# Optimization experiments

Hardware: AMD Instinct MI355X
Metric: run time of the kernel (lower is better)

## Reference

```python
import jax, jax.numpy as jnp
import numpy as np

HEAD_SIZE = 64


def setup_inputs() -> dict:
    key = jax.random.key(0)
    kx, kk, kq, kv = jax.random.split(key, 4)
    B, T, C = 4, 4096, 1024
    x = jax.random.normal(kx, (B, T, C), dtype=jnp.float32)
    Wk = jax.random.normal(kk, (C, HEAD_SIZE), dtype=jnp.float32) * 0.02
    Wq = jax.random.normal(kq, (C, HEAD_SIZE), dtype=jnp.float32) * 0.02
    Wv = jax.random.normal(kv, (C, HEAD_SIZE), dtype=jnp.float32) * 0.02
    return {"x": x, "Wk": Wk, "Wq": Wq, "Wv": Wv}


def reference(x, Wk, Wq, Wv):
    # x: (B,T,C); projections to (B,T,H)
    T = x.shape[1]
    k = jnp.einsum('btc,ch->bth', x, Wk)
    q = jnp.einsum('btc,ch->bth', x, Wq)
    v = jnp.einsum('btc,ch->bth', x, Wv)
    scale = 1.0 / jnp.sqrt(jnp.float32(HEAD_SIZE))
    wei = jnp.einsum('bth,bsh->bts', q, k) * scale  # (B,T,T)
    causal = jnp.tril(jnp.ones((T, T), dtype=bool))
    wei = jnp.where(causal, wei, -jnp.inf)
    wei = jax.nn.softmax(wei, axis=-1)
    out = jnp.einsum('bts,bsh->bth', wei, v)  # (B,T,H)
    return out
```

## Files before the change

kernel.cpp:

```cpp
#include <hip/hip_runtime.h>

typedef __attribute__((ext_vector_type(8))) short short8;
typedef __attribute__((ext_vector_type(4))) float f32x4;
typedef unsigned short u16;

#define BB 4
#define TT 4096
#define CC 1024
#define HH 64

static __device__ __forceinline__ u16 f2bf(float f) {
    unsigned int u = __float_as_uint(f);
    unsigned int r = (u + 0x7FFFu + ((u >> 16) & 1u)) >> 16;
    return (u16)r;
}

static __device__ __forceinline__ unsigned int cvtpk(float lo, float hi) {
    unsigned int r;
    asm("v_cvt_pk_bf16_f32 %0, %1, %2" : "=v"(r) : "v"(lo), "v"(hi));
    return r;
}

static __device__ __forceinline__ int swz(int row, int chunk) {
    return row * 64 + ((chunk ^ (row & 7)) << 3);
}

static __device__ __forceinline__ int probe_isbf(const u16* xu, int tid) {
    int lane = tid & 63;
    int cnt = 0;
    for (int i = lane; i < 1024; i += 64) {
        u16 u = xu[2 * i];
        int e = (u >> 7) & 0xFF;
        cnt += (e >= 100 && e <= 140) ? 1 : 0;
    }
    for (int d = 1; d < 64; d <<= 1) cnt += __shfl_xor(cnt, d);
    return (cnt > 512) ? 1 : 0;
}

__global__ void prep(const void* __restrict__ Wk, const void* __restrict__ Wq,
                     const void* __restrict__ Wv, const u16* __restrict__ xu,
                     u16* __restrict__ Wtp, int* __restrict__ flag) {
    __shared__ int sflag;
    if (threadIdx.x < 64) {
        int f = probe_isbf(xu, threadIdx.x);
        if (threadIdx.x == 0) sflag = f;
    }
    __syncthreads();
    const int isbf = sflag;
    if (blockIdx.x == 0 && threadIdx.x == 0) *flag = isbf;

    int r = blockIdx.x;
    int p = r >> 6;
    int n = r & 63;
    int nt = n >> 4, nl = n & 15;
    const void* W = (p == 0) ? Wq : (p == 1) ? Wk : Wv;
    int k0 = threadIdx.x * 4;
    int kb = k0 >> 6, k2 = (k0 >> 5) & 1, quad = (k0 >> 3) & 3, half = (k0 >> 2) & 1;
    ushort4 v;
    if (isbf) {
        const u16* Wb = (const u16*)W;
        v.x = Wb[(k0 + 0) * HH + n]; v.y = Wb[(k0 + 1) * HH + n];
        v.z = Wb[(k0 + 2) * HH + n]; v.w = Wb[(k0 + 3) * HH + n];
    } else {
        const float* Wf = (const float*)W;
        v.x = f2bf(Wf[(k0 + 0) * HH + n]); v.y = f2bf(Wf[(k0 + 1) * HH + n]);
        v.z = f2bf(Wf[(k0 + 2) * HH + n]); v.w = f2bf(Wf[(k0 + 3) * HH + n]);
    }
    size_t off16 = ((size_t)((p * 4 + nt) * 16 + kb) * 2 + k2) * 64 + quad * 16 + nl;
    *reinterpret_cast<ushort4*>(Wtp + off16 * 8 + half * 4) = v;
}

__global__ __launch_bounds__(256) void qkv_proj(const void* __restrict__ x,
                                                const u16* __restrict__ Wtp,
                                                u16* __restrict__ qo, u16* __restrict__ ko,
                                                u16* __restrict__ vo, const int* __restrict__ flag) {
    __shared__ __align__(16) u16 xs[32 * 1024];
    __shared__ __align__(16) u16 tls[4][3][256];
    const int isbf = *flag;
    const int tid = threadIdx.x;
    const int lane = tid & 63;
    const int w = tid >> 6;
    const int l15 = lane & 15;
    const int quad = lane >> 4;
    int phys = blockIdx.x;
    int rb = (phys & 7) * 64 + (phys >> 3);
    const int g0r = rb * 32;

    #pragma unroll
    for (int j = 0; j < 16; j++) {
        int c = tid + j * 256;
        int row = c >> 7, ck = c & 127;
        int dst = row * 1024 + ((ck ^ (row & 7)) << 3);
        if (isbf) {
            uint4 d = *reinterpret_cast<const uint4*>((const u16*)x + (size_t)(g0r + row) * CC + ck * 8);
            *reinterpret_cast<uint4*>(xs + dst) = d;
        } else {
            const float4* pf = reinterpret_cast<const float4*>((const float*)x + (size_t)(g0r + row) * CC + ck * 8);
            float4 a0 = pf[0], a1 = pf[1];
            ushort4 lo; lo.x = f2bf(a0.x); lo.y = f2bf(a0.y); lo.z = f2bf(a0.z); lo.w = f2bf(a0.w);
            ushort4 hi; hi.x = f2bf(a1.x); hi.y = f2bf(a1.y); hi.z = f2bf(a1.z); hi.w = f2bf(a1.w);
            *reinterpret_cast<ushort4*>(xs + dst) = lo;
            *reinterpret_cast<ushort4*>(xs + dst + 4) = hi;
        }
    }
    __syncthreads();

    f32x4 zero = {0.f, 0.f, 0.f, 0.f};
    f32x4 acc[3][2];
    #pragma unroll
    for (int i = 0; i < 3; i++) { acc[i][0] = zero; acc[i][1] = zero; }

    for (int kb = 0; kb < 16; kb++) {
        #pragma unroll
        for (int k2 = 0; k2 < 2; k2++) {
            int ck = kb * 8 + k2 * 4 + quad;
            int xo = ((ck ^ (l15 & 7)) << 3);
            short8 af0 = *reinterpret_cast<const short8*>(xs + l15 * 1024 + xo);
            short8 af1 = *reinterpret_cast<const short8*>(xs + (16 + l15) * 1024 + xo);
            #pragma unroll
            for (int p = 0; p < 3; p++) {
                short8 bf = *reinterpret_cast<const short8*>(
                    Wtp + ((((size_t)(p * 4 + w) * 16 + kb) * 2 + k2) * 64 + lane) * 8);
                acc[p][0] = __builtin_amdgcn_mfma_f32_16x16x32_bf16(af0, bf, acc[p][0], 0, 0, 0);
                acc[p][1] = __builtin_amdgcn_mfma_f32_16x16x32_bf16(af1, bf, acc[p][1], 0, 0, 0);
            }
        }
    }

    const float qscale = 0.18033688011112042f;
    #pragma unroll
    for (int rt = 0; rt < 2; rt++) {
        const int g0rt = g0r + rt * 16;
        #pragma unroll
        for (int p = 0; p < 3; p++) {
            if (p < 2) {
                float sc = (p == 0) ? qscale : 1.f;
                #pragma unroll
                for (int r = 0; r < 4; r++)
                    tls[w][p][(quad * 4 + r) * 16 + l15] = f2bf(acc[p][rt][r] * sc);
            } else {
                #pragma unroll
                for (int r = 0; r < 4; r++)
                    tls[w][p][l15 * 16 + quad * 4 + r] = f2bf(acc[p][rt][r]);
            }
        }
        #pragma unroll
        for (int p = 0; p < 2; p++) {
            int t = lane >> 2, seg = lane & 3;
            ushort4 d = *reinterpret_cast<const ushort4*>(&tls[w][p][t * 16 + seg * 4]);
            u16* dst = (p == 0) ? qo : ko;
            *reinterpret_cast<ushort4*>(dst + (size_t)(g0rt + t) * HH + w * 16 + seg * 4) = d;
        }
        {
            int c = lane >> 2, seg = lane & 3;
            ushort4 d = *reinterpret_cast<const ushort4*>(&tls[w][2][c * 16 + seg * 4]);
            int b = g0rt >> 12;
            int kt = (g0rt & 4095) >> 6;
            int toff = g0rt & 63;
            *reinterpret_cast<ushort4*>(vo + ((size_t)((b * 64 + kt) * 64 + w * 16 + c)) * 64 + toff + seg * 4) = d;
        }
    }
}

static __device__ __forceinline__ void attn_step(const u16* __restrict__ kstc,
                                                 const u16* __restrict__ vtsc,
                                                 u16* __restrict__ pbw,
                                                 const short8* aq, f32x4* o, float& lsum,
                                                 int kt, int q_g, bool dm, int l15, int quad) {
    f32x4 zero = {0.f, 0.f, 0.f, 0.f};
    f32x4 s[4];
    #pragma unroll
    for (int i = 0; i < 4; i++) s[i] = zero;
    __builtin_amdgcn_s_setprio(1);
    #pragma unroll
    for (int k2 = 0; k2 < 2; k2++) {
        #pragma unroll
        for (int nt = 0; nt < 4; nt++) {
            short8 af = *reinterpret_cast<const short8*>(&kstc[swz(nt * 16 + l15, k2 * 4 + quad)]);
            s[nt] = __builtin_amdgcn_mfma_f32_16x16x32_bf16(af, aq[k2], s[nt], 0, 0, 0);
        }
    }
    __builtin_amdgcn_s_setprio(0);
    #pragma unroll
    for (int nt = 0; nt < 4; nt++) {
        int key0 = kt * 64 + nt * 16 + quad * 4;
        #pragma unroll
        for (int r = 0; r < 4; r++) {
            float pv = __builtin_amdgcn_exp2f(s[nt][r]);
            if (dm && key0 + r > q_g) pv = 0.f;
            s[nt][r] = pv;
        }
    }
    #pragma unroll
    for (int nt = 0; nt < 4; nt++)
        lsum += (s[nt][0] + s[nt][1]) + (s[nt][2] + s[nt][3]);
    #pragma unroll
    for (int nt = 0; nt < 4; nt++) {
        uint2 pk;
        pk.x = cvtpk(s[nt][0], s[nt][1]);
        pk.y = cvtpk(s[nt][2], s[nt][3]);
        int addr = swz(l15, nt * 2 + (quad >> 1)) + (quad & 1) * 4;
        *reinterpret_cast<uint2*>(&pbw[addr]) = pk;
    }
    __builtin_amdgcn_s_setprio(1);
    #pragma unroll
    for (int k2 = 0; k2 < 2; k2++) {
        short8 bp = *reinterpret_cast<const short8*>(&pbw[swz(l15, k2 * 4 + quad)]);
        #pragma unroll
        for (int nt = 0; nt < 4; nt++) {
            short8 av = *reinterpret_cast<const short8*>(&vtsc[swz(nt * 16 + l15, k2 * 4 + quad)]);
            o[nt] = __builtin_amdgcn_mfma_f32_16x16x32_bf16(av, bp, o[nt], 0, 0, 0);
        }
    }
    __builtin_amdgcn_s_setprio(0);
}

__global__ __launch_bounds__(256) void attn(const u16* __restrict__ qp, const u16* __restrict__ kp,
                                            const u16* __restrict__ vp, float* __restrict__ acco,
                                            float* __restrict__ accl, void* __restrict__ outv,
                                            const int* __restrict__ flag, int nsplit) {
    __shared__ __align__(16) u16 kst[2][64 * 64];
    __shared__ __align__(16) u16 vts[2][64 * 64];
    __shared__ __align__(16) u16 pb[4][16 * 64];
    const int isbf = *flag;
    const int tid = threadIdx.x;
    const int lane = tid & 63;
    const int w = tid >> 6;
    const int l15 = lane & 15;
    const int quad = lane >> 4;

    int u = blockIdx.x;
    int per = 32 * nsplit;
    int b = u / per;
    int rem = u - b * per;
    int p = rem / nsplit;
    int ks = rem - p * nsplit;
    const int qtA = 63 - p;
    const int qtB = p;

    const int q_gA = qtA * 64 + w * 16 + l15;
    const int q_gB = qtB * 64 + w * 16 + l15;

    short8 aqA[2], aqB[2];
    {
        const u16* qr = qp + (size_t)(b * TT + q_gA) * HH;
        aqA[0] = *reinterpret_cast<const short8*>(qr + quad * 8);
        aqA[1] = *reinterpret_cast<const short8*>(qr + 32 + quad * 8);
    }
    {
        const u16* qr = qp + (size_t)(b * TT + q_gB) * HH;
        aqB[0] = *reinterpret_cast<const short8*>(qr + quad * 8);
        aqB[1] = *reinterpret_cast<const short8*>(qr + 32 + quad * 8);
    }

    const int cc0 = tid, cc1 = tid + 256;
    const int dst0 = swz(cc0 >> 3, cc0 & 7);
    const int dst1 = swz(cc1 >> 3, cc1 & 7);
    const u16* kbase = kp + (size_t)b * TT * HH;
    const u16* vbase = vp + (size_t)b * 64 * 64 * 64;

    f32x4 zero = {0.f, 0.f, 0.f, 0.f};
    f32x4 oA[4], oB[4];
    #pragma unroll
    for (int i = 0; i < 4; i++) { oA[i] = zero; oB[i] = zero; }
    float lsumA = 0.f, lsumB = 0.f;

    const int nstep = (qtA - ks) / nsplit + 1;

    uint4 rk0, rk1, rv0, rv1;
    {
        size_t t0 = (size_t)ks * 4096;
        rk0 = *reinterpret_cast<const uint4*>(kbase + t0 + cc0 * 8);
        rk1 = *reinterpret_cast<const uint4*>(kbase + t0 + cc1 * 8);
        rv0 = *reinterpret_cast<const uint4*>(vbase + t0 + cc0 * 8);
        rv1 = *reinterpret_cast<const uint4*>(vbase + t0 + cc1 * 8);
    }
    *reinterpret_cast<uint4*>(&kst[0][dst0]) = rk0;
    *reinterpret_cast<uint4*>(&kst[0][dst1]) = rk1;
    *reinterpret_cast<uint4*>(&vts[0][dst0]) = rv0;
    *reinterpret_cast<uint4*>(&vts[0][dst1]) = rv1;
    if (nstep > 1) {
        size_t t1 = (size_t)(ks + nsplit) * 4096;
        rk0 = *reinterpret_cast<const uint4*>(kbase + t1 + cc0 * 8);
        rk1 = *reinterpret_cast<const uint4*>(kbase + t1 + cc1 * 8);
        rv0 = *reinterpret_cast<const uint4*>(vbase + t1 + cc0 * 8);
        rv1 = *reinterpret_cast<const uint4*>(vbase + t1 + cc1 * 8);
    }

    for (int j = 0; j < nstep; ++j) {
        __syncthreads();
        const int cur = j & 1;
        if (j + 1 < nstep) {
            *reinterpret_cast<uint4*>(&kst[cur ^ 1][dst0]) = rk0;
            *reinterpret_cast<uint4*>(&kst[cur ^ 1][dst1]) = rk1;
            *reinterpret_cast<uint4*>(&vts[cur ^ 1][dst0]) = rv0;
            *reinterpret_cast<uint4*>(&vts[cur ^ 1][dst1]) = rv1;
        }
        if (j + 2 < nstep) {
            size_t tn = (size_t)(ks + (j + 2) * nsplit) * 4096;
            rk0 = *reinterpret_cast<const uint4*>(kbase + tn + cc0 * 8);
            rk1 = *reinterpret_cast<const uint4*>(kbase + tn + cc1 * 8);
            rv0 = *reinterpret_cast<const uint4*>(vbase + tn + cc0 * 8);
            rv1 = *reinterpret_cast<const uint4*>(vbase + tn + cc1 * 8);
        }
        const int kt = ks + j * nsplit;
        attn_step(&kst[cur][0], &vts[cur][0], &pb[w][0], aqA, oA, lsumA,
                  kt, q_gA, kt == qtA, l15, quad);
        if (kt <= qtB)
            attn_step(&kst[cur][0], &vts[cur][0], &pb[w][0], aqB, oB, lsumB,
                      kt, q_gB, kt == qtB, l15, quad);
    }

    lsumA += __shfl_xor(lsumA, 16);
    lsumA += __shfl_xor(lsumA, 32);
    lsumB += __shfl_xor(lsumB, 16);
    lsumB += __shfl_xor(lsumB, 32);

    const size_t g0qA = (size_t)(b * TT) + q_gA;
    const size_t g0qB = (size_t)(b * TT) + q_gB;

    if (nsplit == 1) {
        float invA = 1.0f / lsumA;
        float invB = 1.0f / lsumB;
        if (isbf) {
            u16* outp = (u16*)outv;
            #pragma unroll
            for (int nt = 0; nt < 4; nt++) {
                ushort4 sa, sb;
                sa.x = f2bf(oA[nt][0] * invA); sa.y = f2bf(oA[nt][1] * invA);
                sa.z = f2bf(oA[nt][2] * invA); sa.w = f2bf(oA[nt][3] * invA);
                sb.x = f2bf(oB[nt][0] * invB); sb.y = f2bf(oB[nt][1] * invB);
                sb.z = f2bf(oB[nt][2] * invB); sb.w = f2bf(oB[nt][3] * invB);
                *reinterpret_cast<ushort4*>(outp + g0qA * HH + nt * 16 + quad * 4) = sa;
                *reinterpret_cast<ushort4*>(outp + g0qB * HH + nt * 16 + quad * 4) = sb;
            }
        } else {
            float* outp = (float*)outv;
            #pragma unroll
            for (int nt = 0; nt < 4; nt++) {
                float4 sa = {oA[nt][0] * invA, oA[nt][1] * invA, oA[nt][2] * invA, oA[nt][3] * invA};
                float4 sb = {oB[nt][0] * invB, oB[nt][1] * invB, oB[nt][2] * invB, oB[nt][3] * invB};
                *reinterpret_cast<float4*>(outp + g0qA * HH + nt * 16 + quad * 4) = sa;
                *reinterpret_cast<float4*>(outp + g0qB * HH + nt * 16 + quad * 4) = sb;
            }
        }
    } else {
        float* accos = acco + (size_t)ks * (BB * TT * HH);
        float* accls = accl + (size_t)ks * (BB * TT);
        #pragma unroll
        for (int nt = 0; nt < 4; nt++) {
            float4 sv = {oA[nt][0], oA[nt][1], oA[nt][2], oA[nt][3]};
            *reinterpret_cast<float4*>(accos + g0qA * HH + nt * 16 + quad * 4) = sv;
        }
        if (quad == 0) accls[g0qA] = lsumA;
        if (ks <= qtB) {
            #pragma unroll
            for (int nt = 0; nt < 4; nt++) {
                float4 sv = {oB[nt][0], oB[nt][1], oB[nt][2], oB[nt][3]};
                *reinterpret_cast<float4*>(accos + g0qB * HH + nt * 16 + quad * 4) = sv;
            }
            if (quad == 0) accls[g0qB] = lsumB;
        }
    }
}

__global__ __launch_bounds__(256) void attn_finalize(const float* __restrict__ acco,
                                                     const float* __restrict__ accl,
                                                     void* __restrict__ outv,
                                                     const int* __restrict__ flag, int nsplit) {
    const int isbf = *flag;
    int i = blockIdx.x * blockDim.x + threadIdx.x;
    int row = i >> 4;
    int qt = (row & (TT - 1)) >> 6;
    int nact = min(nsplit, qt + 1);
    float4 ov = reinterpret_cast<const float4*>(acco)[i];
    float l = accl[row];
    for (int s = 1; s < nact; s++) {
        float4 t = reinterpret_cast<const float4*>(acco + (size_t)s * (BB * TT * HH))[i];
        ov.x += t.x; ov.y += t.y; ov.z += t.z; ov.w += t.w;
        l += accl[(size_t)s * (BB * TT) + row];
    }
    float inv = 1.0f / l;
    if (isbf) {
        ushort4 s;
        s.x = f2bf(ov.x * inv); s.y = f2bf(ov.y * inv);
        s.z = f2bf(ov.z * inv); s.w = f2bf(ov.w * inv);
        reinterpret_cast<ushort4*>(outv)[i] = s;
    } else {
        float4 s = {ov.x * inv, ov.y * inv, ov.z * inv, ov.w * inv};
        reinterpret_cast<float4*>(outv)[i] = s;
    }
}

extern "C" void kernel_launch(void* const* d_in, const int* in_sizes, int n_in,
                              void* d_out, int out_size, void* d_ws, size_t ws_size,
                              hipStream_t stream) {
    const void* x  = d_in[0];
    const void* Wk = d_in[1];
    const void* Wq = d_in[2];
    const void* Wv = d_in[3];
    char* ws = (char*)d_ws;
    u16* qo = (u16*)(ws);
    u16* ko = (u16*)(ws + (size_t)2 * 1024 * 1024);
    u16* vo = (u16*)(ws + (size_t)4 * 1024 * 1024);
    u16* Wtp = (u16*)(ws + (size_t)6 * 1024 * 1024);
    int* flag = (int*)(ws + (size_t)6 * 1024 * 1024 + 768 * 1024);
    float* acco = (float*)(ws + (size_t)7 * 1024 * 1024);
    float* accl = (float*)(ws + (size_t)39 * 1024 * 1024);

    const size_t need_split = (size_t)40 * 1024 * 1024;
    const int nsplit = (ws_size >= need_split) ? 8 : 1;

    prep<<<192, 256, 0, stream>>>(Wk, Wq, Wv, (const u16*)x, Wtp, flag);
    qkv_proj<<<512, 256, 0, stream>>>(x, Wtp, qo, ko, vo, flag);
    attn<<<BB * 32 * nsplit, 256, 0, stream>>>(qo, ko, vo, acco, accl, d_out, flag, nsplit);
    if (nsplit > 1) {
        attn_finalize<<<(BB * TT * HH / 4) / 256, 256, 0, stream>>>(acco, accl, d_out, flag, nsplit);
    }
}
```

Baseline: 145.9 us.

## Load K fragments directly from global into registers, drop K LDS staging

K tiles are no longer staged through shared memory. Each lane loads its MFMA K fragments straight from global memory into registers and prefetches the next tile's fragments after the QK^T MFMAs. Separate P buffers for the A and B query tiles remove the reuse hazard on the shared P scratch, and the key split factor drops from 8 to 4. This trades LDS traffic and LDS footprint for redundant global/L2 loads of K across the four waves and more register pressure, with fewer, longer split blocks.

```diff
diff --git a/kernel.cpp b/kernel.cpp
--- a/kernel.cpp
+++ b/kernel.cpp
@@ -162,25 +162,29 @@
     }
 }
 
-static __device__ __forceinline__ void attn_step(const u16* __restrict__ kstc,
-                                                 const u16* __restrict__ vtsc,
-                                                 u16* __restrict__ pbw,
-                                                 const short8* aq, f32x4* o, float& lsum,
-                                                 int kt, int q_g, bool dm, int l15, int quad) {
-    f32x4 zero = {0.f, 0.f, 0.f, 0.f};
-    f32x4 s[4];
-    #pragma unroll
-    for (int i = 0; i < 4; i++) s[i] = zero;
+static __device__ __forceinline__ void qkt_regs(const short8* kf, const short8* aq, f32x4* s) {
     __builtin_amdgcn_s_setprio(1);
     #pragma unroll
     for (int k2 = 0; k2 < 2; k2++) {
         #pragma unroll
-        for (int nt = 0; nt < 4; nt++) {
-            short8 af = *reinterpret_cast<const short8*>(&kstc[swz(nt * 16 + l15, k2 * 4 + quad)]);
-            s[nt] = __builtin_amdgcn_mfma_f32_16x16x32_bf16(af, aq[k2], s[nt], 0, 0, 0);
-        }
+        for (int nt = 0; nt < 4; nt++)
+            s[nt] = __builtin_amdgcn_mfma_f32_16x16x32_bf16(kf[k2 * 4 + nt], aq[k2], s[nt], 0, 0, 0);
     }
     __builtin_amdgcn_s_setprio(0);
+}
+
+static __device__ __forceinline__ void load_kf(short8* kf, const u16* kfb, size_t toff) {
+    #pragma unroll
+    for (int k2 = 0; k2 < 2; k2++) {
+        #pragma unroll
+        for (int nt = 0; nt < 4; nt++)
+            kf[k2 * 4 + nt] = *reinterpret_cast<const short8*>(kfb + toff + nt * 1024 + k2 * 32);
+    }
+}
+
+static __device__ __forceinline__ void smpv(f32x4* s, const u16* __restrict__ vtsc,
+                                            u16* __restrict__ pbw, f32x4* o, float& lsum,
+                                            int kt, int q_g, bool dm, int l15, int quad) {
     #pragma unroll
     for (int nt = 0; nt < 4; nt++) {
         int key0 = kt * 64 + nt * 16 + quad * 4;
@@ -219,9 +223,9 @@
                                             const u16* __restrict__ vp, float* __restrict__ acco,
                                             float* __restrict__ accl, void* __restrict__ outv,
                                             const int* __restrict__ flag, int nsplit) {
-    __shared__ __align__(16) u16 kst[2][64 * 64];
     __shared__ __align__(16) u16 vts[2][64 * 64];
-    __shared__ __align__(16) u16 pb[4][16 * 64];
+    __shared__ __align__(16) u16 pba[4][16 * 64];
+    __shared__ __align__(16) u16 pbb[4][16 * 64];
     const int isbf = *flag;
     const int tid = threadIdx.x;
     const int lane = tid & 63;
@@ -256,8 +260,8 @@
     const int cc0 = tid, cc1 = tid + 256;
     const int dst0 = swz(cc0 >> 3, cc0 & 7);
     const int dst1 = swz(cc1 >> 3, cc1 & 7);
-    const u16* kbase = kp + (size_t)b * TT * HH;
     const u16* vbase = vp + (size_t)b * 64 * 64 * 64;
+    const u16* kfb = kp + (size_t)b * TT * HH + l15 * 64 + quad * 8;
 
     f32x4 zero = {0.f, 0.f, 0.f, 0.f};
     f32x4 oA[4], oB[4];
@@ -267,22 +271,18 @@
 
     const int nstep = (qtA - ks) / nsplit + 1;
 
-    uint4 rk0, rk1, rv0, rv1;
+    short8 kf[8];
+    load_kf(kf, kfb, (size_t)ks * 4096);
+    uint4 rv0, rv1;
     {
         size_t t0 = (size_t)ks * 4096;
-        rk0 = *reinterpret_cast<const uint4*>(kbase + t0 + cc0 * 8);
-        rk1 = *reinterpret_cast<const uint4*>(kbase + t0 + cc1 * 8);
         rv0 = *reinterpret_cast<const uint4*>(vbase + t0 + cc0 * 8);
         rv1 = *reinterpret_cast<const uint4*>(vbase + t0 + cc1 * 8);
     }
-    *reinterpret_cast<uint4*>(&kst[0][dst0]) = rk0;
-    *reinterpret_cast<uint4*>(&kst[0][dst1]) = rk1;
     *reinterpret_cast<uint4*>(&vts[0][dst0]) = rv0;
     *reinterpret_cast<uint4*>(&vts[0][dst1]) = rv1;
     if (nstep > 1) {
         size_t t1 = (size_t)(ks + nsplit) * 4096;
-        rk0 = *reinterpret_cast<const uint4*>(kbase + t1 + cc0 * 8);
-        rk1 = *reinterpret_cast<const uint4*>(kbase + t1 + cc1 * 8);
         rv0 = *reinterpret_cast<const uint4*>(vbase + t1 + cc0 * 8);
         rv1 = *reinterpret_cast<const uint4*>(vbase + t1 + cc1 * 8);
     }
@@ -291,24 +291,33 @@
         __syncthreads();
         const int cur = j & 1;
         if (j + 1 < nstep) {
-            *reinterpret_cast<uint4*>(&kst[cur ^ 1][dst0]) = rk0;
-            *reinterpret_cast<uint4*>(&kst[cur ^ 1][dst1]) = rk1;
             *reinterpret_cast<uint4*>(&vts[cur ^ 1][dst0]) = rv0;
             *reinterpret_cast<uint4*>(&vts[cur ^ 1][dst1]) = rv1;
         }
         if (j + 2 < nstep) {
             size_t tn = (size_t)(ks + (j + 2) * nsplit) * 4096;
-            rk0 = *reinterpret_cast<const uint4*>(kbase + tn + cc0 * 8);
-            rk1 = *reinterpret_cast<const uint4*>(kbase + tn + cc1 * 8);
             rv0 = *reinterpret_cast<const uint4*>(vbase + tn + cc0 * 8);
             rv1 = *reinterpret_cast<const uint4*>(vbase + tn + cc1 * 8);
         }
         const int kt = ks + j * nsplit;
-        attn_step(&kst[cur][0], &vts[cur][0], &pb[w][0], aqA, oA, lsumA,
-                  kt, q_gA, kt == qtA, l15, quad);
-        if (kt <= qtB)
-            attn_step(&kst[cur][0], &vts[cur][0], &pb[w][0], aqB, oB, lsumB,
-                      kt, q_gB, kt == qtB, l15, quad);
+        const bool doB = (kt <= qtB);
+        const size_t tnext = (size_t)(kt + nsplit) * 4096;
+
+        f32x4 sA[4];
+        #pragma unroll
+        for (int i = 0; i < 4; i++) sA[i] = zero;
+        qkt_regs(kf, aqA, sA);
+        if (!doB && j + 1 < nstep) load_kf(kf, kfb, tnext);
+        smpv(sA, &vts[cur][0], &pba[w][0], oA, lsumA, kt, q_gA, kt == qtA, l15, quad);
+
+        if (doB) {
+            f32x4 sB[4];
+            #pragma unroll
+            for (int i = 0; i < 4; i++) sB[i] = zero;
+            qkt_regs(kf, aqB, sB);
+            if (j + 1 < nstep) load_kf(kf, kfb, tnext);
+            smpv(sB, &vts[cur][0], &pbb[w][0], oB, lsumB, kt, q_gB, kt == qtB, l15, quad);
+        }
     }
 
     lsumA += __shfl_xor(lsumA, 16);
@@ -409,7 +418,7 @@
     float* accl = (float*)(ws + (size_t)39 * 1024 * 1024);
 
     const size_t need_split = (size_t)40 * 1024 * 1024;
-    const int nsplit = (ws_size >= need_split) ? 8 : 1;
+    const int nsplit = (ws_size >= need_split) ? 4 : 1;
 
     prep<<<192, 256, 0, stream>>>(Wk, Wq, Wv, (const u16*)x, Wtp, flag);
     qkv_proj<<<512, 256, 0, stream>>>(x, Wtp, qo, ko, vo, flag);
```

New measurement: 155.1 us. +6.3%, slower.
